# Kernel tuning notes

Hardware: AMD Instinct MI355X
Metric: run time of the kernel (lower is better)

## Reference

```python
import jax, jax.numpy as jnp
import numpy as np

N_CANONICAL = 16
D_IN, D_HID, D_OUT = 784, 128, 10
BATCH = 65536


def setup_inputs() -> dict:
    key = jax.random.key(0)
    ks = jax.random.split(key, 6)
    x = jax.random.normal(ks[0], (BATCH, D_IN), dtype=jnp.float32)
    # per-canonical Linear params (PyTorch Linear: y = x @ W.T + b)
    s1 = 1.0 / np.sqrt(D_IN)
    s2 = 1.0 / np.sqrt(D_HID)
    fc_w = jax.random.uniform(ks[1], (N_CANONICAL, D_HID, D_IN), jnp.float32, -s1, s1)
    fc_b = jax.random.uniform(ks[2], (N_CANONICAL, D_HID), jnp.float32, -s1, s1)
    cls_w = jax.random.uniform(ks[3], (N_CANONICAL, D_OUT, D_HID), jnp.float32, -s2, s2)
    cls_b = jax.random.uniform(ks[4], (N_CANONICAL, D_OUT), jnp.float32, -s2, s2)
    factor = jnp.full((N_CANONICAL,), 1.0 / N_CANONICAL, dtype=jnp.float32)
    return {"x": x, "fc_w": fc_w, "fc_b": fc_b, "cls_w": cls_w, "cls_b": cls_b, "factor": factor}


def reference(x, fc_w, fc_b, cls_w, cls_b, factor):
    # x: [B, 784] (already flattened view of 28x28)
    # Ensemble of Linears combined by learned scalar factor. Since the combination
    # is linear, pre-combine weights: sum_k factor[k] * W_k (same math, fused GEMM).
    w1 = jnp.einsum('k,kod->od', factor, fc_w)   # [128, 784]
    b1 = factor @ fc_b                           # [128]
    h = jax.nn.relu(x @ w1.T + b1)               # [B, 128]
    w2 = jnp.einsum('k,kod->od', factor, cls_w)  # [10, 128]
    b2 = factor @ cls_b                          # [10]
    out = h @ w2.T + b2                          # [B, 10]
    return out
```

## Files before the change

kernel.cpp:

```cpp
#include <hip/hip_runtime.h>
#include <hip/hip_bf16.h>

typedef __attribute__((ext_vector_type(8))) short short8;
typedef __attribute__((ext_vector_type(4))) float f32x4;

#define N_ENS 16
#define D_IN 784
#define D_HID 128
#define D_OUT 10
#define KPAD 800
#define NKT 25
#define TILE_B 8192
#define WS_B1 204800
#define WS_W2 205312
#define WS_B2 210432

__device__ __forceinline__ unsigned short f2bf(float f) {
  unsigned int u = __float_as_uint(f);
  return (unsigned short)((u + 0x7FFFu + ((u >> 16) & 1u)) >> 16);
}

__device__ __forceinline__ void gload_lds16(const void* g, void* l) {
  __builtin_amdgcn_global_load_lds((const __attribute__((address_space(1))) void*)g,
                                   (__attribute__((address_space(3))) void*)l, 16, 0, 0);
}

__device__ __forceinline__ int bswz(int c, int kg) {
  return ((c >> 1) << 7) + (((((c & 1) << 2) | kg) ^ ((c >> 1) & 7)) << 4);
}

__global__ void prep_kernel(const float* __restrict__ fc_w, const float* __restrict__ fc_b,
                            const float* __restrict__ cls_w, const float* __restrict__ cls_b,
                            const float* __restrict__ factor, char* __restrict__ ws) {
  int tid = blockIdx.x * 256 + threadIdx.x;
  float f[N_ENS];
#pragma unroll
  for (int e = 0; e < N_ENS; ++e) f[e] = factor[e];

  if (tid < 25600) {
    int col = tid / 200;
    int kq  = tid - col * 200;
    int k   = kq * 4;
    float4 v = float4{0.f, 0.f, 0.f, 0.f};
    if (k + 3 < D_IN) {
#pragma unroll
      for (int e = 0; e < N_ENS; ++e) {
        const float4 t = *(const float4*)(fc_w + (size_t)(e * D_HID + col) * D_IN + k);
        v.x += f[e] * t.x; v.y += f[e] * t.y; v.z += f[e] * t.z; v.w += f[e] * t.w;
      }
    }
    const int kt = k >> 5, kg = (k & 31) >> 3, half = k & 7;
    union { unsigned short u[4]; uint2 p; } pk;
    pk.u[0] = f2bf(v.x); pk.u[1] = f2bf(v.y); pk.u[2] = f2bf(v.z); pk.u[3] = f2bf(v.w);
    *(uint2*)(ws + kt * TILE_B + bswz(col, kg) + half * 2) = pk.p;
  } else if (tid < 25600 + D_HID) {
    int col = tid - 25600;
    float v = 0.f;
#pragma unroll
    for (int e = 0; e < N_ENS; ++e) v += f[e] * fc_b[e * D_HID + col];
    *(float*)(ws + WS_B1 + col * 4) = v;
  } else if (tid < 25600 + D_HID + D_HID * D_OUT) {
    int i = tid - (25600 + D_HID);
    int o = i >> 7, n = i & 127;
    float v = 0.f;
#pragma unroll
    for (int e = 0; e < N_ENS; ++e) v += f[e] * cls_w[(e * D_OUT + o) * D_HID + n];
    *(float*)(ws + WS_W2 + i * 4) = v;
  } else if (tid < 25600 + D_HID + D_HID * D_OUT + D_OUT) {
    int o = tid - (25600 + D_HID + D_HID * D_OUT);
    float v = 0.f;
#pragma unroll
    for (int e = 0; e < N_ENS; ++e) v += f[e] * cls_b[e * D_OUT + o];
    *(float*)(ws + WS_B2 + o * 4) = v;
  }
}

__global__ __launch_bounds__(256, 4) void mnist_fused(const float* __restrict__ x,
                                                      const char* __restrict__ ws,
                                                      float* __restrict__ out) {
  __shared__ __align__(16) char smem[38912];
  const int tid  = threadIdx.x;
  const int lane = tid & 63;
  const int w    = tid >> 6;
  const int l15  = lane & 15;
  const int kg   = lane >> 4;
  const int m0   = blockIdx.x * 64;

  const float* ar = x + (size_t)(m0 + w * 16 + l15) * D_IN;
  int boff[8];
#pragma unroll
  for (int ni = 0; ni < 8; ++ni) boff[ni] = bswz(ni * 16 + l15, kg);

  f32x4 acc[8];
#pragma unroll
  for (int ni = 0; ni < 8; ++ni) acc[ni] = f32x4{0.f, 0.f, 0.f, 0.f};

  gload_lds16(ws + w * 2048 + lane * 16,        smem + w * 2048);
  gload_lds16(ws + w * 2048 + 1024 + lane * 16, smem + w * 2048 + 1024);
  float4 a0 = *(const float4*)(ar + kg * 8);
  float4 a1 = *(const float4*)(ar + kg * 8 + 4);

  for (int kt = 0; kt < NKT; ++kt) {
    const int cur = kt & 1;
    const int ktn = kt + 1;
    if (ktn < NKT) {
      const char* src = ws + ktn * TILE_B + w * 2048;
      char* dst = smem + (ktn & 1) * 8192 + w * 2048;
      gload_lds16(src + lane * 16, dst);
      gload_lds16(src + 1024 + lane * 16, dst + 1024);
    }
    union { unsigned short u[8]; short8 s; } pk;
    pk.u[0] = f2bf(a0.x); pk.u[1] = f2bf(a0.y); pk.u[2] = f2bf(a0.z); pk.u[3] = f2bf(a0.w);
    pk.u[4] = f2bf(a1.x); pk.u[5] = f2bf(a1.y); pk.u[6] = f2bf(a1.z); pk.u[7] = f2bf(a1.w);
    if (ktn < NKT) {
      if (ktn < 24 || kg < 2) {
        a0 = *(const float4*)(ar + ktn * 32 + kg * 8);
        a1 = *(const float4*)(ar + ktn * 32 + kg * 8 + 4);
      } else {
        a0 = float4{0.f, 0.f, 0.f, 0.f};
        a1 = float4{0.f, 0.f, 0.f, 0.f};
      }
      __builtin_amdgcn_sched_barrier(0);
      asm volatile("s_waitcnt vmcnt(4)" ::: "memory");
      __builtin_amdgcn_sched_barrier(0);
    } else {
      __builtin_amdgcn_sched_barrier(0);
      asm volatile("s_waitcnt vmcnt(0)" ::: "memory");
      __builtin_amdgcn_sched_barrier(0);
    }
    __builtin_amdgcn_s_barrier();
    __builtin_amdgcn_sched_barrier(0);
    {
      const char* Bb = smem + cur * 8192;
      short8 b[8];
#pragma unroll
      for (int ni = 0; ni < 8; ++ni) b[ni] = *(const short8*)(Bb + boff[ni]);
#pragma unroll
      for (int ni = 0; ni < 8; ++ni)
        acc[ni] = __builtin_amdgcn_mfma_f32_16x16x32_bf16(pk.s, b[ni], acc[ni], 0, 0, 0);
    }
    __builtin_amdgcn_sched_barrier(0);
    __builtin_amdgcn_s_barrier();
    __builtin_amdgcn_sched_barrier(0);
  }

  __syncthreads();

  const float* b1g = (const float*)(ws + WS_B1);
  float (*h)[132] = (float (*)[132])smem;
#pragma unroll
  for (int ni = 0; ni < 8; ++ni) {
    const float bv = b1g[ni * 16 + l15];
#pragma unroll
    for (int j = 0; j < 4; ++j) {
      float v = acc[ni][j] + bv;
      h[w * 16 + kg * 4 + j][ni * 16 + l15] = v > 0.f ? v : 0.f;
    }
  }
  float* w2s = (float*)(smem + 33792);
  {
    const float* w2g = (const float*)(ws + WS_W2);
    for (int i = tid; i < 1280; i += 256) w2s[i] = w2g[i];
  }
  __syncthreads();

  const int row = w * 16 + l15;
  float po[10];
#pragma unroll
  for (int o = 0; o < 10; ++o) po[o] = 0.f;
#pragma unroll
  for (int n4 = 0; n4 < 8; ++n4) {
    const float4 hv = *(const float4*)(&h[row][kg * 32 + n4 * 4]);
#pragma unroll
    for (int o = 0; o < 10; ++o) {
      const float4 wv = *(const float4*)(w2s + o * 128 + kg * 32 + n4 * 4);
      po[o] += hv.x * wv.x + hv.y * wv.y + hv.z * wv.z + hv.w * wv.w;
    }
  }
#pragma unroll
  for (int o = 0; o < 10; ++o) {
    po[o] += __shfl_xor(po[o], 16);
    po[o] += __shfl_xor(po[o], 32);
  }
  if (kg == 0) {
    const float* b2g = (const float*)(ws + WS_B2);
    float* op = out + (size_t)(m0 + row) * 10;
#pragma unroll
    for (int o = 0; o < 10; o += 2) {
      float2 v;
      v.x = po[o]     + b2g[o];
      v.y = po[o + 1] + b2g[o + 1];
      *(float2*)(op + o) = v;
    }
  }
}

extern "C" void kernel_launch(void* const* d_in, const int* in_sizes, int n_in,
                              void* d_out, int out_size, void* d_ws, size_t ws_size,
                              hipStream_t stream) {
  const float* x      = (const float*)d_in[0];
  const float* fc_w   = (const float*)d_in[1];
  const float* fc_b   = (const float*)d_in[2];
  const float* cls_w  = (const float*)d_in[3];
  const float* cls_b  = (const float*)d_in[4];
  const float* factor = (const float*)d_in[5];
  char* ws = (char*)d_ws;
  float* outp = (float*)d_out;

  prep_kernel<<<106, 256, 0, stream>>>(fc_w, fc_b, cls_w, cls_b, factor, ws);
  mnist_fused<<<1024, 256, 0, stream>>>(x, ws, outp);
}
```

Before: 49.37 us.

## Triple-buffer weight tiles and prefetch activations two K-steps ahead

The main GEMM loop moves from double-buffered LDS weight tiles with a one-step prefetch to three rotating LDS buffers and two register sets for the x tiles. Both the weight tiles and the activations are prefetched two iterations ahead, and the loop is manually unrolled by two. The goal is to keep more global loads in flight so the bandwidth-bound stream of x hides latency better. The cost is extra LDS (still inside the existing buffer) and more live registers, which could affect the four-blocks-per-CU occupancy target.

```diff
diff --git a/kernel.cpp b/kernel.cpp
--- a/kernel.cpp
+++ b/kernel.cpp
@@ -8,7 +8,6 @@
 #define D_IN 784
 #define D_HID 128
 #define D_OUT 10
-#define KPAD 800
 #define NKT 25
 #define TILE_B 8192
 #define WS_B1 204800
@@ -74,6 +73,9 @@
     *(float*)(ws + WS_B2 + o * 4) = v;
   }
 }
+
+#define SB __builtin_amdgcn_sched_barrier(0)
+#define ROT(o) o = ((o) == 16384) ? 0 : (o) + 8192
 
 __global__ __launch_bounds__(256, 4) void mnist_fused(const float* __restrict__ x,
                                                       const char* __restrict__ ws,
@@ -95,54 +97,60 @@
 #pragma unroll
   for (int ni = 0; ni < 8; ++ni) acc[ni] = f32x4{0.f, 0.f, 0.f, 0.f};
 
-  gload_lds16(ws + w * 2048 + lane * 16,        smem + w * 2048);
-  gload_lds16(ws + w * 2048 + 1024 + lane * 16, smem + w * 2048 + 1024);
-  float4 a0 = *(const float4*)(ar + kg * 8);
-  float4 a1 = *(const float4*)(ar + kg * 8 + 4);
-
-  for (int kt = 0; kt < NKT; ++kt) {
-    const int cur = kt & 1;
-    const int ktn = kt + 1;
-    if (ktn < NKT) {
-      const char* src = ws + ktn * TILE_B + w * 2048;
-      char* dst = smem + (ktn & 1) * 8192 + w * 2048;
-      gload_lds16(src + lane * 16, dst);
-      gload_lds16(src + 1024 + lane * 16, dst + 1024);
-    }
-    union { unsigned short u[8]; short8 s; } pk;
-    pk.u[0] = f2bf(a0.x); pk.u[1] = f2bf(a0.y); pk.u[2] = f2bf(a0.z); pk.u[3] = f2bf(a0.w);
-    pk.u[4] = f2bf(a1.x); pk.u[5] = f2bf(a1.y); pk.u[6] = f2bf(a1.z); pk.u[7] = f2bf(a1.w);
-    if (ktn < NKT) {
-      if (ktn < 24 || kg < 2) {
-        a0 = *(const float4*)(ar + ktn * 32 + kg * 8);
-        a1 = *(const float4*)(ar + ktn * 32 + kg * 8 + 4);
-      } else {
-        a0 = float4{0.f, 0.f, 0.f, 0.f};
-        a1 = float4{0.f, 0.f, 0.f, 0.f};
-      }
-      __builtin_amdgcn_sched_barrier(0);
-      asm volatile("s_waitcnt vmcnt(4)" ::: "memory");
-      __builtin_amdgcn_sched_barrier(0);
-    } else {
-      __builtin_amdgcn_sched_barrier(0);
-      asm volatile("s_waitcnt vmcnt(0)" ::: "memory");
-      __builtin_amdgcn_sched_barrier(0);
-    }
-    __builtin_amdgcn_s_barrier();
-    __builtin_amdgcn_sched_barrier(0);
-    {
-      const char* Bb = smem + cur * 8192;
-      short8 b[8];
-#pragma unroll
-      for (int ni = 0; ni < 8; ++ni) b[ni] = *(const short8*)(Bb + boff[ni]);
-#pragma unroll
-      for (int ni = 0; ni < 8; ++ni)
-        acc[ni] = __builtin_amdgcn_mfma_f32_16x16x32_bf16(pk.s, b[ni], acc[ni], 0, 0, 0);
-    }
-    __builtin_amdgcn_sched_barrier(0);
-    __builtin_amdgcn_s_barrier();
-    __builtin_amdgcn_sched_barrier(0);
-  }
+  gload_lds16(ws + w * 2048 + lane * 16,                 smem + w * 2048);
+  gload_lds16(ws + w * 2048 + 1024 + lane * 16,          smem + w * 2048 + 1024);
+  gload_lds16(ws + TILE_B + w * 2048 + lane * 16,        smem + 8192 + w * 2048);
+  gload_lds16(ws + TILE_B + w * 2048 + 1024 + lane * 16, smem + 8192 + w * 2048 + 1024);
+  float4 aA0 = *(const float4*)(ar + kg * 8);
+  float4 aA1 = *(const float4*)(ar + kg * 8 + 4);
+  float4 aB0 = *(const float4*)(ar + 32 + kg * 8);
+  float4 aB1 = *(const float4*)(ar + 32 + kg * 8 + 4);
+
+  int rdoff = 0, wroff = 16384;
+
+#define ITER(kt, A0v, A1v) do {                                               \
+    if ((kt) < 23) { SB; asm volatile("s_waitcnt vmcnt(4)" ::: "memory"); SB; }\
+    else           { SB; asm volatile("s_waitcnt vmcnt(0)" ::: "memory"); SB; }\
+    __builtin_amdgcn_s_barrier();       \
+    SB;                                                                        \
+    if ((kt) + 2 < NKT) {                    \
+      const char* src = ws + ((kt) + 2) * TILE_B + w * 2048;                   \
+      char* dst = smem + wroff + w * 2048;                                     \
+      gload_lds16(src + lane * 16, dst);                                       \
+      gload_lds16(src + 1024 + lane * 16, dst + 1024);                         \
+    }                                                                          \
+    union { unsigned short u[8]; short8 s; } pk;            \
+    pk.u[0]=f2bf(A0v.x); pk.u[1]=f2bf(A0v.y); pk.u[2]=f2bf(A0v.z); pk.u[3]=f2bf(A0v.w); \
+    pk.u[4]=f2bf(A1v.x); pk.u[5]=f2bf(A1v.y); pk.u[6]=f2bf(A1v.z); pk.u[7]=f2bf(A1v.w); \
+    if ((kt) + 2 < NKT) {        \
+      if ((kt) + 2 < 24 || kg < 2) {                                           \
+        A0v = *(const float4*)(ar + ((kt) + 2) * 32 + kg * 8);                 \
+        A1v = *(const float4*)(ar + ((kt) + 2) * 32 + kg * 8 + 4);             \
+      } else {                                                                 \
+        A0v = float4{0.f, 0.f, 0.f, 0.f};                                      \
+        A1v = float4{0.f, 0.f, 0.f, 0.f};                                      \
+      }                                                                        \
+    }                                                                          \
+    {                                                                          \
+      const char* Bb = smem + rdoff;                                           \
+      short8 b[8];                                                             \
+      _Pragma("unroll") for (int ni = 0; ni < 8; ++ni)                         \
+        b[ni] = *(const short8*)(Bb + boff[ni]);                               \
+      _Pragma("unroll") for (int ni = 0; ni < 8; ++ni)                         \
+        acc[ni] = __builtin_amdgcn_mfma_f32_16x16x32_bf16(pk.s, b[ni], acc[ni], 0, 0, 0); \
+    }                                                                          \
+    SB;                                                                        \
+    __builtin_amdgcn_s_barrier();                  \
+    SB;                                                                        \
+    ROT(rdoff); ROT(wroff);                                                    \
+  } while (0)
+
+  for (int kt = 0; kt < 24; kt += 2) {
+    ITER(kt,     aA0, aA1);
+    ITER(kt + 1, aB0, aB1);
+  }
+  ITER(24, aA0, aA1);
+#undef ITER
 
   __syncthreads();
 
```

New measurement: 50.31 us. No clear change (+1.9%).

## Stage full bf16 x tile in LDS and split hidden dim across waves

Applied to the files above, without the earlier changes.

Each block now handles 32 rows instead of 64. It first loads the whole 32x784 x tile with coalesced float4 reads, converts it to bf16 and stores it in LDS. The weight tiles are triple-buffered and each wave computes a 32x32 slice of the hidden layer with a 2x2 MFMA tile. The second layer adds a cross-thread LDS reduction, and the grid doubles to 2048 blocks. This is meant to replace strided per-row global reads of x and cut B-fragment traffic per wave, at the cost of much more LDS (about 76KB, so occupancy drops to 2 blocks per CU), a serial x-load phase before any compute, and an extra synchronisation in the epilogue.

```diff
diff --git a/kernel.cpp b/kernel.cpp
--- a/kernel.cpp
+++ b/kernel.cpp
@@ -8,12 +8,15 @@
 #define D_IN 784
 #define D_HID 128
 #define D_OUT 10
-#define KPAD 800
 #define NKT 25
 #define TILE_B 8192
 #define WS_B1 204800
 #define WS_W2 205312
 #define WS_B2 210432
+
+#define A_STRIDE 1616
+#define B_BASE 51712
+#define SB __builtin_amdgcn_sched_barrier(0)
 
 __device__ __forceinline__ unsigned short f2bf(float f) {
   unsigned int u = __float_as_uint(f);
@@ -75,73 +78,93 @@
   }
 }
 
-__global__ __launch_bounds__(256, 4) void mnist_fused(const float* __restrict__ x,
+__global__ __launch_bounds__(256, 2) void mnist_fused(const float* __restrict__ x,
                                                       const char* __restrict__ ws,
                                                       float* __restrict__ out) {
-  __shared__ __align__(16) char smem[38912];
+  __shared__ __align__(16) char smem[76288];
   const int tid  = threadIdx.x;
   const int lane = tid & 63;
   const int w    = tid >> 6;
   const int l15  = lane & 15;
   const int kg   = lane >> 4;
-  const int m0   = blockIdx.x * 64;
-
-  const float* ar = x + (size_t)(m0 + w * 16 + l15) * D_IN;
-  int boff[8];
-#pragma unroll
-  for (int ni = 0; ni < 8; ++ni) boff[ni] = bswz(ni * 16 + l15, kg);
-
-  f32x4 acc[8];
-#pragma unroll
-  for (int ni = 0; ni < 8; ++ni) acc[ni] = f32x4{0.f, 0.f, 0.f, 0.f};
-
-  gload_lds16(ws + w * 2048 + lane * 16,        smem + w * 2048);
-  gload_lds16(ws + w * 2048 + 1024 + lane * 16, smem + w * 2048 + 1024);
-  float4 a0 = *(const float4*)(ar + kg * 8);
-  float4 a1 = *(const float4*)(ar + kg * 8 + 4);
-
+  const int m0   = blockIdx.x * 32;
+
+  char* Bb = smem + B_BASE;
+
+  gload_lds16(ws + w * 2048 + lane * 16,                 Bb + w * 2048);
+  gload_lds16(ws + w * 2048 + 1024 + lane * 16,          Bb + w * 2048 + 1024);
+  gload_lds16(ws + TILE_B + w * 2048 + lane * 16,        Bb + 8192 + w * 2048);
+  gload_lds16(ws + TILE_B + w * 2048 + 1024 + lane * 16, Bb + 8192 + w * 2048 + 1024);
+
+  {
+    const float* xb = x + (size_t)m0 * D_IN;
+#pragma unroll 6
+    for (int i = 0; i < 24; ++i) {
+      const int g   = i * 256 + tid;
+      const int row = g / 196;
+      const int c4  = g - row * 196;
+      const float4 v = *(const float4*)(xb + row * D_IN + c4 * 4);
+      union { unsigned short u[4]; uint2 p; } pk;
+      pk.u[0] = f2bf(v.x); pk.u[1] = f2bf(v.y); pk.u[2] = f2bf(v.z); pk.u[3] = f2bf(v.w);
+      *(uint2*)(smem + row * A_STRIDE + c4 * 8) = pk.p;
+    }
+    if (tid < 128) {
+      const int c4 = 68 + tid;
+      const float4 v = *(const float4*)(xb + 31 * D_IN + c4 * 4);
+      union { unsigned short u[4]; uint2 p; } pk;
+      pk.u[0] = f2bf(v.x); pk.u[1] = f2bf(v.y); pk.u[2] = f2bf(v.z); pk.u[3] = f2bf(v.w);
+      *(uint2*)(smem + 31 * A_STRIDE + c4 * 8) = pk.p;
+    }
+    if (tid < 128) {
+      const int row = tid >> 2, c4 = 196 + (tid & 3);
+      *(uint2*)(smem + row * A_STRIDE + c4 * 8) = uint2{0u, 0u};
+    }
+  }
+  __syncthreads();
+
+  int aoff[2];
+#pragma unroll
+  for (int mi = 0; mi < 2; ++mi) aoff[mi] = (mi * 16 + l15) * A_STRIDE + kg * 16;
+  int boff[2];
+#pragma unroll
+  for (int ni = 0; ni < 2; ++ni) boff[ni] = bswz(w * 32 + ni * 16 + l15, kg);
+
+  f32x4 acc[2][2];
+#pragma unroll
+  for (int mi = 0; mi < 2; ++mi)
+#pragma unroll
+    for (int ni = 0; ni < 2; ++ni) acc[mi][ni] = f32x4{0.f, 0.f, 0.f, 0.f};
+
+  int rdoff = 0, wroff = 16384;
   for (int kt = 0; kt < NKT; ++kt) {
-    const int cur = kt & 1;
-    const int ktn = kt + 1;
-    if (ktn < NKT) {
-      const char* src = ws + ktn * TILE_B + w * 2048;
-      char* dst = smem + (ktn & 1) * 8192 + w * 2048;
+    if (kt <= 22) {
+      const char* src = ws + (kt + 2) * TILE_B + w * 2048;
+      char* dst = Bb + wroff + w * 2048;
       gload_lds16(src + lane * 16, dst);
       gload_lds16(src + 1024 + lane * 16, dst + 1024);
-    }
-    union { unsigned short u[8]; short8 s; } pk;
-    pk.u[0] = f2bf(a0.x); pk.u[1] = f2bf(a0.y); pk.u[2] = f2bf(a0.z); pk.u[3] = f2bf(a0.w);
-    pk.u[4] = f2bf(a1.x); pk.u[5] = f2bf(a1.y); pk.u[6] = f2bf(a1.z); pk.u[7] = f2bf(a1.w);
-    if (ktn < NKT) {
-      if (ktn < 24 || kg < 2) {
-        a0 = *(const float4*)(ar + ktn * 32 + kg * 8);
-        a1 = *(const float4*)(ar + ktn * 32 + kg * 8 + 4);
-      } else {
-        a0 = float4{0.f, 0.f, 0.f, 0.f};
-        a1 = float4{0.f, 0.f, 0.f, 0.f};
-      }
-      __builtin_amdgcn_sched_barrier(0);
-      asm volatile("s_waitcnt vmcnt(4)" ::: "memory");
-      __builtin_amdgcn_sched_barrier(0);
+      SB; asm volatile("s_waitcnt vmcnt(4)" ::: "memory"); SB;
+    } else if (kt == 23) {
+      SB; asm volatile("s_waitcnt vmcnt(2)" ::: "memory"); SB;
     } else {
-      __builtin_amdgcn_sched_barrier(0);
-      asm volatile("s_waitcnt vmcnt(0)" ::: "memory");
-      __builtin_amdgcn_sched_barrier(0);
+      SB; asm volatile("s_waitcnt vmcnt(0)" ::: "memory"); SB;
     }
     __builtin_amdgcn_s_barrier();
-    __builtin_amdgcn_sched_barrier(0);
-    {
-      const char* Bb = smem + cur * 8192;
-      short8 b[8];
-#pragma unroll
-      for (int ni = 0; ni < 8; ++ni) b[ni] = *(const short8*)(Bb + boff[ni]);
-#pragma unroll
-      for (int ni = 0; ni < 8; ++ni)
-        acc[ni] = __builtin_amdgcn_mfma_f32_16x16x32_bf16(pk.s, b[ni], acc[ni], 0, 0, 0);
-    }
-    __builtin_amdgcn_sched_barrier(0);
+    SB;
+    short8 a[2], b[2];
+#pragma unroll
+    for (int mi = 0; mi < 2; ++mi) a[mi] = *(const short8*)(smem + aoff[mi] + kt * 64);
+#pragma unroll
+    for (int ni = 0; ni < 2; ++ni) b[ni] = *(const short8*)(Bb + rdoff + boff[ni]);
+#pragma unroll
+    for (int mi = 0; mi < 2; ++mi)
+#pragma unroll
+      for (int ni = 0; ni < 2; ++ni)
+        acc[mi][ni] = __builtin_amdgcn_mfma_f32_16x16x32_bf16(a[mi], b[ni], acc[mi][ni], 0, 0, 0);
+    SB;
     __builtin_amdgcn_s_barrier();
-    __builtin_amdgcn_sched_barrier(0);
+    SB;
+    rdoff = (rdoff == 16384) ? 0 : rdoff + 8192;
+    wroff = (wroff == 16384) ? 0 : wroff + 8192;
   }
 
   __syncthreads();
@@ -149,49 +172,49 @@
   const float* b1g = (const float*)(ws + WS_B1);
   float (*h)[132] = (float (*)[132])smem;
 #pragma unroll
-  for (int ni = 0; ni < 8; ++ni) {
-    const float bv = b1g[ni * 16 + l15];
-#pragma unroll
-    for (int j = 0; j < 4; ++j) {
-      float v = acc[ni][j] + bv;
-      h[w * 16 + kg * 4 + j][ni * 16 + l15] = v > 0.f ? v : 0.f;
-    }
-  }
-  float* w2s = (float*)(smem + 33792);
+  for (int ni = 0; ni < 2; ++ni) {
+    const float bv = b1g[w * 32 + ni * 16 + l15];
+#pragma unroll
+    for (int mi = 0; mi < 2; ++mi) {
+#pragma unroll
+      for (int j = 0; j < 4; ++j) {
+        float v = acc[mi][ni][j] + bv;
+        h[mi * 16 + kg * 4 + j][w * 32 + ni * 16 + l15] = v > 0.f ? v : 0.f;
+      }
+    }
+  }
+  float* red = (float*)(smem + B_BASE);
+  float* w2s = (float*)(smem + B_BASE + 10240);
   {
     const float* w2g = (const float*)(ws + WS_W2);
     for (int i = tid; i < 1280; i += 256) w2s[i] = w2g[i];
   }
   __syncthreads();
 
-  const int row = w * 16 + l15;
+  const int r = tid & 31, q = tid >> 5;
   float po[10];
 #pragma unroll
   for (int o = 0; o < 10; ++o) po[o] = 0.f;
 #pragma unroll
-  for (int n4 = 0; n4 < 8; ++n4) {
-    const float4 hv = *(const float4*)(&h[row][kg * 32 + n4 * 4]);
+  for (int j4 = 0; j4 < 4; ++j4) {
+    const float4 hv = *(const float4*)(&h[r][q * 16 + j4 * 4]);
 #pragma unroll
     for (int o = 0; o < 10; ++o) {
-      const float4 wv = *(const float4*)(w2s + o * 128 + kg * 32 + n4 * 4);
+      const float4 wv = *(const float4*)(w2s + o * 128 + q * 16 + j4 * 4);
       po[o] += hv.x * wv.x + hv.y * wv.y + hv.z * wv.z + hv.w * wv.w;
     }
   }
 #pragma unroll
-  for (int o = 0; o < 10; ++o) {
-    po[o] += __shfl_xor(po[o], 16);
-    po[o] += __shfl_xor(po[o], 32);
-  }
-  if (kg == 0) {
+  for (int o = 0; o < 10; ++o) red[(q * 32 + r) * 10 + o] = po[o];
+  __syncthreads();
+
+  for (int i = tid; i < 320; i += 256) {
+    const int rr = i / 10, o = i - rr * 10;
     const float* b2g = (const float*)(ws + WS_B2);
-    float* op = out + (size_t)(m0 + row) * 10;
-#pragma unroll
-    for (int o = 0; o < 10; o += 2) {
-      float2 v;
-      v.x = po[o]     + b2g[o];
-      v.y = po[o + 1] + b2g[o + 1];
-      *(float2*)(op + o) = v;
-    }
+    float s = b2g[o];
+#pragma unroll
+    for (int qq = 0; qq < 8; ++qq) s += red[(qq * 32 + rr) * 10 + o];
+    out[(size_t)(m0 + rr) * 10 + o] = s;
   }
 }
 
@@ -208,5 +231,5 @@
   float* outp = (float*)d_out;
 
   prep_kernel<<<106, 256, 0, stream>>>(fc_w, fc_b, cls_w, cls_b, factor, ws);
-  mnist_fused<<<1024, 256, 0, stream>>>(x, ws, outp);
-}
+  mnist_fused<<<2048, 256, 0, stream>>>(x, ws, outp);
+}
```

Measured after the change: 72.05 us. 1.46x slower.
